# Performance work log

Measured on AMD Instinct MI355X. Metric: run time of the kernel, lower is better.

## Reference

```python
import jax, jax.numpy as jnp
import numpy as np

N_LAYERS = 4
D_MODEL = 1024
HEADS = 16
D_HEAD = D_MODEL // HEADS
SEQ = 1024
VOCAB = 512
FF = 4 * D_MODEL
MEM_LEN = 512
CMEM_LEN = 128
MAX_KLEN = SEQ + MEM_LEN + CMEM_LEN
BATCH = 4
LN_EPS = 1e-5
NEG = -1000000000.0


def shift(x):
    # Music-Transformer skew trick, faithful to torch shift()
    *lead, i, j = x.shape
    x = jnp.concatenate([x, jnp.zeros((*lead, i, i), x.dtype)], axis=-1)
    l = i + j - 1
    x = x.reshape(*lead, -1)
    pad = (-x.shape[-1]) % l
    x = jnp.concatenate([x, jnp.zeros((*lead, pad), x.dtype)], axis=-1)
    x = x.reshape(*lead, -1, l)
    return x[..., :i, i - 1:]


def layer_norm(x, g, b):
    mu = jnp.mean(x, axis=-1, keepdims=True)
    var = jnp.mean(jnp.square(x - mu), axis=-1, keepdims=True)
    return (x - mu) * jax.lax.rsqrt(var + LN_EPS) * g + b


def setup_inputs() -> dict:
    key = jax.random.key(0)
    ks = jax.random.split(key, 12)
    s = 0.02
    return {
        'seq': jax.random.randint(ks[0], (BATCH, SEQ), 0, VOCAB),
        'mask': jnp.ones((BATCH, SEQ), dtype=bool),
        'cmems': jnp.zeros((N_LAYERS, BATCH, CMEM_LEN, D_MODEL), jnp.float32),
        'mems': jnp.zeros((N_LAYERS, BATCH, MEM_LEN, D_MODEL), jnp.float32),
        'embed': jax.random.normal(ks[1], (VOCAB, D_MODEL), jnp.float32) * s,
        'Wq': jax.random.normal(ks[2], (N_LAYERS, D_MODEL, D_MODEL), jnp.float32) * s,
        'Wk': jax.random.normal(ks[3], (N_LAYERS, D_MODEL, D_MODEL), jnp.float32) * s,
        'Wv': jax.random.normal(ks[4], (N_LAYERS, D_MODEL, D_MODEL), jnp.float32) * s,
        'Wo': jax.random.normal(ks[5], (N_LAYERS, D_MODEL, D_MODEL), jnp.float32) * s,
        'r_emb': jax.random.normal(ks[6], (N_LAYERS, HEADS, MAX_KLEN, D_HEAD), jnp.float32) * s,
        'r_w_bias': jax.random.normal(ks[7], (N_LAYERS, HEADS, D_HEAD), jnp.float32) * s,
        'r_bias': jax.random.normal(ks[8], (N_LAYERS, HEADS, MAX_KLEN), jnp.float32) * s,
        'ln1_g': jnp.ones((N_LAYERS, D_MODEL), jnp.float32),
        'ln1_b': jnp.zeros((N_LAYERS, D_MODEL), jnp.float32),
        'ln2_g': jnp.ones((N_LAYERS, D_MODEL), jnp.float32),
        'ln2_b': jnp.zeros((N_LAYERS, D_MODEL), jnp.float32),
        'w1': jax.random.normal(ks[9], (N_LAYERS, FF, D_MODEL), jnp.float32) * s,
        'b1': jnp.zeros((N_LAYERS, FF), jnp.float32),
        'w2': jax.random.normal(ks[10], (N_LAYERS, D_MODEL, FF), jnp.float32) * s,
        'b2': jnp.zeros((N_LAYERS, D_MODEL), jnp.float32),
    }


def reference(seq, mask, cmems, mems, embed, Wq, Wk, Wv, Wo, r_emb,
              r_w_bias, r_bias, ln1_g, ln1_b, ln2_g, ln2_b, w1, b1, w2, b2):
    # Note: Encoder.forward passes memories=None to each layer, so cmems/mems
    # are unused, ar_loss == 0, and k_len == seq_len (faithful to source).
    B, S = seq.shape
    x = embed[seq]  # [B, S, D]
    # mask: [B,S] -> pairwise [B,1,S,S]
    m4 = (mask[:, :, None] & mask[:, None, :])[:, None]
    scale = HEADS ** -0.5  # source uses 1/sqrt(h), not 1/sqrt(d_head)

    def heads_split(y):  # [B,S,D] -> [B,H,S,dh]
        return y.reshape(B, S, HEADS, D_HEAD).transpose(0, 2, 1, 3)

    for i in range(N_LAYERS):
        q = heads_split(x @ Wq[i].T)
        k = heads_split(x @ Wk[i].T)
        v = heads_split(x @ Wv[i].T)
        re = r_emb[i][:, -S:, :]    # [H, S, dh]
        rb = r_bias[i][:, -S:]      # [H, S]
        r_query = q + r_w_bias[i][None, :, None, :]
        AC = jnp.einsum('bhid,bhjd->bhij', r_query, k)
        B_ = jnp.einsum('bhid,hjd->bhij', q, re)
        BD = shift(B_ + rb[None, :, None, :])
        score = (AC + BD) * scale
        score = jnp.where(m4, score, NEG)
        attn = jax.nn.softmax(score, axis=-1)
        out = jnp.einsum('bhij,bhjd->bhid', attn, v)
        out = out.transpose(0, 2, 1, 3).reshape(B, S, D_MODEL) @ Wo[i].T
        x = layer_norm(x + out, ln1_g[i], ln1_b[i])
        ff = jax.nn.gelu(x @ w1[i].T + b1[i], approximate=False) @ w2[i].T + b2[i]
        x = layer_norm(x + ff, ln2_g[i], ln2_b[i])
    return x
```

## Files before the change

kernel.cpp:

```cpp
#include <hip/hip_runtime.h>
#include <stdint.h>

#define DM 1024
#define NH 16
#define DH 64
#define SQ 1024
#define NB 4
#define FFD 4096
#define MAXK 1664
#define ROWS 4096
#define L2E 1.4426950408889634f

typedef __attribute__((ext_vector_type(8))) short short8;
typedef __attribute__((ext_vector_type(4))) float f32x4;

static __device__ __forceinline__ unsigned short f2bf(float f) {
    unsigned u = __float_as_uint(f);
    return (unsigned short)((u + 0x7fffu + ((u >> 16) & 1u)) >> 16);
}
static __device__ __forceinline__ float bf2f(unsigned short s) {
    return __uint_as_float(((unsigned)s) << 16);
}

__global__ __launch_bounds__(256) void k_embed(const int* __restrict__ seq,
                                               const float* __restrict__ emb,
                                               float* __restrict__ x,
                                               unsigned short* __restrict__ xb) {
    const int row = blockIdx.x, t = threadIdx.x;
    const int tok = seq[row];
    const float4 v = *(const float4*)(emb + (long)tok * DM + t * 4);
    *(float4*)(x + (long)row * DM + t * 4) = v;
    ushort4 o; o.x = f2bf(v.x); o.y = f2bf(v.y); o.z = f2bf(v.z); o.w = f2bf(v.w);
    *(ushort4*)(xb + (long)row * DM + t * 4) = o;
}

__global__ __launch_bounds__(256) void k_reb(const float* __restrict__ re,
                                             unsigned short* __restrict__ reb) {
    const long e = ((long)blockIdx.x * 256 + threadIdx.x) * 4;
    const int d = (int)(e & 63);
    const long rem = e >> 6;
    const int j = (int)(rem & 1023);
    const long lh = rem >> 10;
    const float4 v = *(const float4*)(re + (lh * MAXK + 640 + j) * DH + d);
    ushort4 o; o.x = f2bf(v.x); o.y = f2bf(v.y); o.z = f2bf(v.z); o.w = f2bf(v.w);
    *(ushort4*)(reb + e) = o;
}

__global__ __launch_bounds__(256) void k_ln(float* __restrict__ x,
                                            unsigned short* __restrict__ xb,
                                            const float* __restrict__ gw,
                                            const float* __restrict__ bw) {
    const int row = blockIdx.x, t = threadIdx.x;
    float4 v = *(const float4*)(x + (long)row * DM + t * 4);
    float s = v.x + v.y + v.z + v.w;
    float sq = v.x * v.x + v.y * v.y + v.z * v.z + v.w * v.w;
#pragma unroll
    for (int mk = 1; mk < 64; mk <<= 1) { s += __shfl_xor(s, mk); sq += __shfl_xor(sq, mk); }
    __shared__ float red[8];
    if ((t & 63) == 0) { red[(t >> 6) * 2] = s; red[(t >> 6) * 2 + 1] = sq; }
    __syncthreads();
    const float ts = red[0] + red[2] + red[4] + red[6];
    const float tq = red[1] + red[3] + red[5] + red[7];
    const float mu = ts * (1.f / DM);
    const float rstd = rsqrtf(tq * (1.f / DM) - mu * mu + 1e-5f);
    const float4 g4 = *(const float4*)(gw + t * 4);
    const float4 b4 = *(const float4*)(bw + t * 4);
    float4 o;
    o.x = (v.x - mu) * rstd * g4.x + b4.x;
    o.y = (v.y - mu) * rstd * g4.y + b4.y;
    o.z = (v.z - mu) * rstd * g4.z + b4.z;
    o.w = (v.w - mu) * rstd * g4.w + b4.w;
    *(float4*)(x + (long)row * DM + t * 4) = o;
    ushort4 ob; ob.x = f2bf(o.x); ob.y = f2bf(o.y); ob.z = f2bf(o.z); ob.w = f2bf(o.w);
    *(ushort4*)(xb + (long)row * DM + t * 4) = ob;
}

template <int MT, int EPI>
__global__ __launch_bounds__(256) void k_gemm(
    const unsigned short* __restrict__ A,
    const float* __restrict__ B0, const float* __restrict__ B1, const float* __restrict__ B2,
    const int K, const int N,
    float* __restrict__ xres, const float* __restrict__ bias,
    unsigned short* __restrict__ d0, unsigned short* __restrict__ d1,
    unsigned short* __restrict__ d2) {
    constexpr int BMv = MT * 32;
    __shared__ unsigned short As[BMv * 40];
    __shared__ unsigned short Bs[128 * 40];
    const int t = threadIdx.x;
    const int w = t >> 6, l = t & 63, g = l >> 4, c = l & 15;
    const int z = blockIdx.z;
    const float* Bw = (z == 0) ? B0 : ((z == 1) ? B1 : B2);
    const long m0 = (long)blockIdx.y * BMv, n0 = (long)blockIdx.x * 128;
    const int arow = (MT == 4) ? (t >> 1) : (t >> 2);
    const int aseg = (MT == 4) ? ((t & 1) * 16) : ((t & 3) * 8);
    const int brow = t >> 1, bseg = (t & 1) * 16;
    const unsigned short* asrc = A + (m0 + arow) * K + aseg;
    const float* bsrc = Bw + (n0 + brow) * K + bseg;
    f32x4 acc[MT][4];
#pragma unroll
    for (int i = 0; i < MT; i++)
#pragma unroll
        for (int j = 0; j < 4; j++) acc[i][j] = (f32x4){0.f, 0.f, 0.f, 0.f};
    const int wr = (w >> 1) * (MT * 16), wc = (w & 1) * 64;

    for (int kt = 0; kt < K; kt += 32) {
        uint4 a0, a1;
        a0 = *(const uint4*)(asrc + kt);
        if constexpr (MT == 4) a1 = *(const uint4*)(asrc + kt + 8);
        float4 f0 = *(const float4*)(bsrc + kt);
        float4 f1 = *(const float4*)(bsrc + kt + 4);
        float4 f2 = *(const float4*)(bsrc + kt + 8);
        float4 f3 = *(const float4*)(bsrc + kt + 12);
        *(uint4*)&As[arow * 40 + aseg] = a0;
        if constexpr (MT == 4) *(uint4*)&As[arow * 40 + aseg + 8] = a1;
        ushort4 u0, u1, u2, u3;
        u0.x = f2bf(f0.x); u0.y = f2bf(f0.y); u0.z = f2bf(f0.z); u0.w = f2bf(f0.w);
        u1.x = f2bf(f1.x); u1.y = f2bf(f1.y); u1.z = f2bf(f1.z); u1.w = f2bf(f1.w);
        u2.x = f2bf(f2.x); u2.y = f2bf(f2.y); u2.z = f2bf(f2.z); u2.w = f2bf(f2.w);
        u3.x = f2bf(f3.x); u3.y = f2bf(f3.y); u3.z = f2bf(f3.z); u3.w = f2bf(f3.w);
        *(ushort4*)&Bs[brow * 40 + bseg] = u0;
        *(ushort4*)&Bs[brow * 40 + bseg + 4] = u1;
        *(ushort4*)&Bs[brow * 40 + bseg + 8] = u2;
        *(ushort4*)&Bs[brow * 40 + bseg + 12] = u3;
        __syncthreads();
        short8 aF[MT], bF[4];
#pragma unroll
        for (int i = 0; i < MT; i++) aF[i] = *(const short8*)&As[(wr + i * 16 + c) * 40 + g * 8];
#pragma unroll
        for (int j = 0; j < 4; j++) bF[j] = *(const short8*)&Bs[(wc + j * 16 + c) * 40 + g * 8];
#pragma unroll
        for (int i = 0; i < MT; i++)
#pragma unroll
            for (int j = 0; j < 4; j++)
                acc[i][j] = __builtin_amdgcn_mfma_f32_16x16x32_bf16(aF[i], bF[j], acc[i][j], 0, 0, 0);
        __syncthreads();
    }

#pragma unroll
    for (int i = 0; i < MT; i++) {
#pragma unroll
        for (int j = 0; j < 4; j++) {
            const long ncol = n0 + wc + j * 16 + c;
            float bval = 0.f;
            if (EPI != 0) bval = (bias != nullptr) ? bias[ncol] : 0.f;
#pragma unroll
            for (int r = 0; r < 4; r++) {
                const long mrow = m0 + wr + i * 16 + g * 4 + r;
                const float vv = acc[i][j][r];
                if (EPI == 0) {
                    const long bb = mrow >> 10, ss = mrow & 1023, hh = ncol >> 6, dd = ncol & 63;
                    if (z == 0)      d0[((bb * NH + hh) * SQ + ss) * DH + dd] = f2bf(vv);
                    else if (z == 1) d1[((bb * NH + hh) * SQ + ss) * DH + dd] = f2bf(vv);
                    else             d2[((bb * NH + hh) * DH + dd) * SQ + ss] = f2bf(vv);
                } else if (EPI == 1) {
                    xres[mrow * DM + ncol] += vv + bval;
                } else {
                    const float xg = vv + bval;
                    d0[mrow * (long)N + ncol] = f2bf(0.5f * xg * (1.f + erff(xg * 0.70710678118654752f)));
                }
            }
        }
    }
}

__global__ __launch_bounds__(256) void k_attn(
    const unsigned short* __restrict__ q, const unsigned short* __restrict__ k,
    const unsigned short* __restrict__ vt, const unsigned short* __restrict__ reb,
    const float* __restrict__ rb, const float* __restrict__ rwb,
    unsigned short* __restrict__ ao) {
    const int t = threadIdx.x, w = t >> 6, l = t & 63, g = l >> 4, c = l & 15;
    const int bh = blockIdx.x, b = bh >> 4, h = bh & 15;
    const int q_base = blockIdx.y * 64 + w * 16;

    __shared__ float rb_s[SQ];
    __shared__ unsigned short p_s[4][640];
    for (int i = t; i < SQ; i += 256) rb_s[i] = rb[h * MAXK + 640 + i];
    __syncthreads();

    const unsigned short* qp = q + ((long)bh * SQ + q_base) * DH;
    const unsigned short* kp = k + (long)bh * SQ * DH;
    const unsigned short* vp = vt + (long)bh * DH * SQ;
    const unsigned short* rp = reb + (long)h * SQ * DH;

    short8 qf[2], qrf[2];
#pragma unroll
    for (int kk = 0; kk < 2; kk++) {
        qf[kk] = *(const short8*)(qp + c * DH + kk * 32 + g * 8);
        short8 tmp;
#pragma unroll
        for (int e = 0; e < 8; e++) {
            float vq = bf2f((unsigned short)qf[kk][e]) + rwb[h * DH + kk * 32 + g * 8 + e];
            tmp[e] = (short)f2bf(vq);
        }
        qrf[kk] = tmp;
    }

    f32x4 O[4];
    float mrow[4], lrow[4];
#pragma unroll
    for (int r = 0; r < 4; r++) { mrow[r] = -1e30f; lrow[r] = 0.f; }
#pragma unroll
    for (int dt = 0; dt < 4; dt++) O[dt] = (f32x4){0.f, 0.f, 0.f, 0.f};

    for (int kt = 0; kt < SQ / 32; kt++) {
        const int k0 = kt * 32;
        f32x4 ac[2];
#pragma unroll
        for (int tt = 0; tt < 2; tt++) {
            short8 kf0 = *(const short8*)(kp + (k0 + tt * 16 + c) * DH + g * 8);
            short8 kf1 = *(const short8*)(kp + (k0 + tt * 16 + c) * DH + 32 + g * 8);
            f32x4 zz = (f32x4){0.f, 0.f, 0.f, 0.f};
            zz = __builtin_amdgcn_mfma_f32_16x16x32_bf16(qrf[0], kf0, zz, 0, 0, 0);
            zz = __builtin_amdgcn_mfma_f32_16x16x32_bf16(qrf[1], kf1, zz, 0, 0, 0);
            ac[tt] = zz;
        }
        const int jb = k0 - q_base + SQ - 16;
        f32x4 G[3];
#pragma unroll
        for (int t2 = 0; t2 < 3; t2++) {
            int jr = jb + t2 * 16 + c;
            int jcl = jr < 0 ? 0 : (jr > SQ - 1 ? SQ - 1 : jr);
            short8 g0 = *(const short8*)(rp + (long)jcl * DH + g * 8);
            short8 g1 = *(const short8*)(rp + (long)jcl * DH + 32 + g * 8);
            f32x4 zz = (f32x4){0.f, 0.f, 0.f, 0.f};
            zz = __builtin_amdgcn_mfma_f32_16x16x32_bf16(qf[0], g0, zz, 0, 0, 0);
            zz = __builtin_amdgcn_mfma_f32_16x16x32_bf16(qf[1], g1, zz, 0, 0, 0);
            const float rbv = rb_s[jcl];
#pragma unroll
            for (int r = 0; r < 4; r++) zz[r] += rbv;
            G[t2] = zz;
        }
        float sc[2][4];
#pragma unroll
        for (int tt = 0; tt < 2; tt++) {
#pragma unroll
            for (int r = 0; r < 4; r++) {
                const int qi = g * 4 + r;
                const int ki = tt * 16 + c;
                const int mm = ki - qi + 15;
                const int sl = (l & 48) | (mm & 15);
                const float glo = __shfl(G[tt][r], sl, 64);
                const float ghi = __shfl(G[tt + 1][r], sl, 64);
                const float gsel = ((mm >> 4) == tt) ? glo : ghi;
                const bool valid = (k0 + ki) <= (q_base + qi);
                sc[tt][r] = (ac[tt][r] + (valid ? gsel : 0.f)) * 0.25f;
            }
        }
        float corr[4];
#pragma unroll
        for (int r = 0; r < 4; r++) {
            float v = fmaxf(sc[0][r], sc[1][r]);
            v = fmaxf(v, __shfl_xor(v, 1)); v = fmaxf(v, __shfl_xor(v, 2));
            v = fmaxf(v, __shfl_xor(v, 4)); v = fmaxf(v, __shfl_xor(v, 8));
            const float mn = fmaxf(mrow[r], v);
            corr[r] = exp2f((mrow[r] - mn) * L2E);
            const float p0 = exp2f((sc[0][r] - mn) * L2E);
            const float p1 = exp2f((sc[1][r] - mn) * L2E);
            float ps = p0 + p1;
            ps += __shfl_xor(ps, 1); ps += __shfl_xor(ps, 2);
            ps += __shfl_xor(ps, 4); ps += __shfl_xor(ps, 8);
            lrow[r] = lrow[r] * corr[r] + ps;
            mrow[r] = mn;
            p_s[w][(g * 4 + r) * 40 + c] = f2bf(p0);
            p_s[w][(g * 4 + r) * 40 + 16 + c] = f2bf(p1);
        }
#pragma unroll
        for (int dt = 0; dt < 4; dt++)
#pragma unroll
            for (int r = 0; r < 4; r++) O[dt][r] *= corr[r];
        __syncthreads();
        const short8 pf = *(const short8*)&p_s[w][c * 40 + g * 8];
#pragma unroll
        for (int dt = 0; dt < 4; dt++) {
            short8 vf = *(const short8*)(vp + (dt * 16 + c) * SQ + k0 + g * 8);
            O[dt] = __builtin_amdgcn_mfma_f32_16x16x32_bf16(pf, vf, O[dt], 0, 0, 0);
        }
    }

#pragma unroll
    for (int r = 0; r < 4; r++) {
        const float rl = 1.f / lrow[r];
        const int s = q_base + g * 4 + r;
#pragma unroll
        for (int dt = 0; dt < 4; dt++) {
            ao[((long)(b * SQ + s)) * DM + h * DH + dt * 16 + c] = f2bf(O[dt][r] * rl);
        }
    }
}

extern "C" void kernel_launch(void* const* d_in, const int* in_sizes, int n_in,
                              void* d_out, int out_size, void* d_ws, size_t ws_size,
                              hipStream_t stream) {
    const int* seq = (const int*)d_in[0];
    const float* emb = (const float*)d_in[4];
    const float* Wq = (const float*)d_in[5];
    const float* Wk = (const float*)d_in[6];
    const float* Wv = (const float*)d_in[7];
    const float* Wo = (const float*)d_in[8];
    const float* remb = (const float*)d_in[9];
    const float* rwb = (const float*)d_in[10];
    const float* rbias = (const float*)d_in[11];
    const float* ln1g = (const float*)d_in[12];
    const float* ln1b = (const float*)d_in[13];
    const float* ln2g = (const float*)d_in[14];
    const float* ln2b = (const float*)d_in[15];
    const float* w1 = (const float*)d_in[16];
    const float* b1 = (const float*)d_in[17];
    const float* w2 = (const float*)d_in[18];
    const float* b2 = (const float*)d_in[19];

    float* x = (float*)d_out;
    char* ws = (char*)d_ws;
    unsigned short* xb  = (unsigned short*)(ws);
    unsigned short* qb  = (unsigned short*)(ws + (8l  << 20));
    unsigned short* kb  = (unsigned short*)(ws + (16l << 20));
    unsigned short* vtb = (unsigned short*)(ws + (24l << 20));
    unsigned short* aob = (unsigned short*)(ws + (32l << 20));
    unsigned short* rebb = (unsigned short*)(ws + (40l << 20));
    unsigned short* hbb = (unsigned short*)(ws + (48l << 20));

    k_embed<<<dim3(ROWS), dim3(256), 0, stream>>>(seq, emb, x, xb);
    k_reb<<<dim3(4096), dim3(256), 0, stream>>>(remb, rebb);

    for (int i = 0; i < 4; i++) {
        const long wOff = (long)i * DM * DM;
        k_gemm<2, 0><<<dim3(8, 64, 3), dim3(256), 0, stream>>>(
            xb, Wq + wOff, Wk + wOff, Wv + wOff, DM, DM, nullptr, nullptr, qb, kb, vtb);
        k_attn<<<dim3(64, 16), dim3(256), 0, stream>>>(
            qb, kb, vtb, rebb + (long)i * NH * SQ * DH, rbias + (long)i * NH * MAXK,
            rwb + (long)i * NH * DH, aob);
        k_gemm<2, 1><<<dim3(8, 64, 1), dim3(256), 0, stream>>>(
            aob, Wo + wOff, nullptr, nullptr, DM, DM, x, nullptr, nullptr, nullptr, nullptr);
        k_ln<<<dim3(ROWS), dim3(256), 0, stream>>>(x, xb, ln1g + i * DM, ln1b + i * DM);
        k_gemm<4, 2><<<dim3(32, 32, 1), dim3(256), 0, stream>>>(
            xb, w1 + (long)i * FFD * DM, nullptr, nullptr, DM, FFD, nullptr,
            b1 + (long)i * FFD, hbb, nullptr, nullptr);
        k_gemm<2, 1><<<dim3(8, 64, 1), dim3(256), 0, stream>>>(
            hbb, w2 + (long)i * DM * FFD, nullptr, nullptr, FFD, DM, x,
            b2 + (long)i * DM, nullptr, nullptr, nullptr);
        k_ln<<<dim3(ROWS), dim3(256), 0, stream>>>(x, xb, ln2g + i * DM, ln2b + i * DM);
    }
}
```

Measured before the change: 2.766 ms.

## Pre-convert weights to bf16, use direct-to-LDS GEMM loads, widen attention tiles

Weights are converted to bf16 in separate kernels before each GEMM, and the fp32 weight conversion is removed from the GEMM inner loop. The GEMM now uses a uniform 128x128 tile and loads A and B with global_load_lds straight into unpadded shared memory. The attention kernel processes 64 keys per iteration instead of 32 and drops a block-wide barrier before reading P. The extra conversion launches and unpadded LDS rows can add traffic and bank conflicts. Workspace buffers are reused for the converted weights, which relies on the order of kernels on the stream.

```diff
diff --git a/kernel.cpp b/kernel.cpp
--- a/kernel.cpp
+++ b/kernel.cpp
@@ -13,6 +13,7 @@
 
 typedef __attribute__((ext_vector_type(8))) short short8;
 typedef __attribute__((ext_vector_type(4))) float f32x4;
+typedef unsigned int u32;
 
 static __device__ __forceinline__ unsigned short f2bf(float f) {
     unsigned u = __float_as_uint(f);
@@ -20,6 +21,10 @@
 }
 static __device__ __forceinline__ float bf2f(unsigned short s) {
     return __uint_as_float(((unsigned)s) << 16);
+}
+static __device__ __forceinline__ void gl16(const void* g, void* l) {
+    __builtin_amdgcn_global_load_lds((const __attribute__((address_space(1))) u32*)g,
+                                     (__attribute__((address_space(3))) u32*)l, 16, 0, 0);
 }
 
 __global__ __launch_bounds__(256) void k_embed(const int* __restrict__ seq,
@@ -44,6 +49,32 @@
     const float4 v = *(const float4*)(re + (lh * MAXK + 640 + j) * DH + d);
     ushort4 o; o.x = f2bf(v.x); o.y = f2bf(v.y); o.z = f2bf(v.z); o.w = f2bf(v.w);
     *(ushort4*)(reb + e) = o;
+}
+
+__global__ __launch_bounds__(256) void k_cvt(const float* __restrict__ s,
+                                             unsigned short* __restrict__ d, int n) {
+    const long i = ((long)blockIdx.x * 256 + threadIdx.x) * 8;
+    if (i >= n) return;
+    const float4 a = *(const float4*)(s + i);
+    const float4 b = *(const float4*)(s + i + 4);
+    ushort4 o0, o1;
+    o0.x = f2bf(a.x); o0.y = f2bf(a.y); o0.z = f2bf(a.z); o0.w = f2bf(a.w);
+    o1.x = f2bf(b.x); o1.y = f2bf(b.y); o1.z = f2bf(b.z); o1.w = f2bf(b.w);
+    *(ushort4*)(d + i) = o0; *(ushort4*)(d + i + 4) = o1;
+}
+__global__ __launch_bounds__(256) void k_cvt3(const float* __restrict__ s0,
+                                              const float* __restrict__ s1,
+                                              const float* __restrict__ s2,
+                                              unsigned short* __restrict__ d) {
+    const float* s = (blockIdx.z == 0) ? s0 : ((blockIdx.z == 1) ? s1 : s2);
+    const long i = ((long)blockIdx.x * 256 + threadIdx.x) * 8;
+    const float4 a = *(const float4*)(s + i);
+    const float4 b = *(const float4*)(s + i + 4);
+    ushort4 o0, o1;
+    o0.x = f2bf(a.x); o0.y = f2bf(a.y); o0.z = f2bf(a.z); o0.w = f2bf(a.w);
+    o1.x = f2bf(b.x); o1.y = f2bf(b.y); o1.z = f2bf(b.z); o1.w = f2bf(b.w);
+    unsigned short* dz = d + (long)blockIdx.z * (DM * DM);
+    *(ushort4*)(dz + i) = o0; *(ushort4*)(dz + i + 4) = o1;
 }
 
 __global__ __launch_bounds__(256) void k_ln(float* __restrict__ x,
@@ -75,61 +106,50 @@
     *(ushort4*)(xb + (long)row * DM + t * 4) = ob;
 }
 
-template <int MT, int EPI>
+template <int EPI>
 __global__ __launch_bounds__(256) void k_gemm(
-    const unsigned short* __restrict__ A,
-    const float* __restrict__ B0, const float* __restrict__ B1, const float* __restrict__ B2,
+    const unsigned short* __restrict__ A, const unsigned short* __restrict__ B,
     const int K, const int N,
     float* __restrict__ xres, const float* __restrict__ bias,
     unsigned short* __restrict__ d0, unsigned short* __restrict__ d1,
     unsigned short* __restrict__ d2) {
-    constexpr int BMv = MT * 32;
-    __shared__ unsigned short As[BMv * 40];
-    __shared__ unsigned short Bs[128 * 40];
+    __shared__ unsigned short As[128 * 32];
+    __shared__ unsigned short Bs[128 * 32];
     const int t = threadIdx.x;
     const int w = t >> 6, l = t & 63, g = l >> 4, c = l & 15;
     const int z = blockIdx.z;
-    const float* Bw = (z == 0) ? B0 : ((z == 1) ? B1 : B2);
-    const long m0 = (long)blockIdx.y * BMv, n0 = (long)blockIdx.x * 128;
-    const int arow = (MT == 4) ? (t >> 1) : (t >> 2);
-    const int aseg = (MT == 4) ? ((t & 1) * 16) : ((t & 3) * 8);
-    const int brow = t >> 1, bseg = (t & 1) * 16;
-    const unsigned short* asrc = A + (m0 + arow) * K + aseg;
-    const float* bsrc = Bw + (n0 + brow) * K + bseg;
-    f32x4 acc[MT][4];
-#pragma unroll
-    for (int i = 0; i < MT; i++)
+    const unsigned short* Bw = B + (long)z * ((long)N * K);
+    const long m0 = (long)blockIdx.y * 128, n0 = (long)blockIdx.x * 128;
+    const int lrow = l >> 2, lseg = (l & 3) << 3;
+    const unsigned short* ag0 = A + (m0 + (w * 2 + 0) * 16 + lrow) * (long)K + lseg;
+    const unsigned short* ag1 = A + (m0 + (w * 2 + 1) * 16 + lrow) * (long)K + lseg;
+    const unsigned short* bg0 = Bw + (n0 + (w * 2 + 0) * 16 + lrow) * (long)K + lseg;
+    const unsigned short* bg1 = Bw + (n0 + (w * 2 + 1) * 16 + lrow) * (long)K + lseg;
+    unsigned short* al0 = &As[(w * 2 + 0) * 512];
+    unsigned short* al1 = &As[(w * 2 + 1) * 512];
+    unsigned short* bl0 = &Bs[(w * 2 + 0) * 512];
+    unsigned short* bl1 = &Bs[(w * 2 + 1) * 512];
+
+    f32x4 acc[4][4];
+#pragma unroll
+    for (int i = 0; i < 4; i++)
 #pragma unroll
         for (int j = 0; j < 4; j++) acc[i][j] = (f32x4){0.f, 0.f, 0.f, 0.f};
-    const int wr = (w >> 1) * (MT * 16), wc = (w & 1) * 64;
+    const int wr = (w >> 1) * 64, wc = (w & 1) * 64;
 
     for (int kt = 0; kt < K; kt += 32) {
-        uint4 a0, a1;
-        a0 = *(const uint4*)(asrc + kt);
-        if constexpr (MT == 4) a1 = *(const uint4*)(asrc + kt + 8);
-        float4 f0 = *(const float4*)(bsrc + kt);
-        float4 f1 = *(const float4*)(bsrc + kt + 4);
-        float4 f2 = *(const float4*)(bsrc + kt + 8);
-        float4 f3 = *(const float4*)(bsrc + kt + 12);
-        *(uint4*)&As[arow * 40 + aseg] = a0;
-        if constexpr (MT == 4) *(uint4*)&As[arow * 40 + aseg + 8] = a1;
-        ushort4 u0, u1, u2, u3;
-        u0.x = f2bf(f0.x); u0.y = f2bf(f0.y); u0.z = f2bf(f0.z); u0.w = f2bf(f0.w);
-        u1.x = f2bf(f1.x); u1.y = f2bf(f1.y); u1.z = f2bf(f1.z); u1.w = f2bf(f1.w);
-        u2.x = f2bf(f2.x); u2.y = f2bf(f2.y); u2.z = f2bf(f2.z); u2.w = f2bf(f2.w);
-        u3.x = f2bf(f3.x); u3.y = f2bf(f3.y); u3.z = f2bf(f3.z); u3.w = f2bf(f3.w);
-        *(ushort4*)&Bs[brow * 40 + bseg] = u0;
-        *(ushort4*)&Bs[brow * 40 + bseg + 4] = u1;
-        *(ushort4*)&Bs[brow * 40 + bseg + 8] = u2;
-        *(ushort4*)&Bs[brow * 40 + bseg + 12] = u3;
+        gl16(ag0 + kt, al0);
+        gl16(ag1 + kt, al1);
+        gl16(bg0 + kt, bl0);
+        gl16(bg1 + kt, bl1);
         __syncthreads();
-        short8 aF[MT], bF[4];
-#pragma unroll
-        for (int i = 0; i < MT; i++) aF[i] = *(const short8*)&As[(wr + i * 16 + c) * 40 + g * 8];
-#pragma unroll
-        for (int j = 0; j < 4; j++) bF[j] = *(const short8*)&Bs[(wc + j * 16 + c) * 40 + g * 8];
-#pragma unroll
-        for (int i = 0; i < MT; i++)
+        short8 aF[4], bF[4];
+#pragma unroll
+        for (int i = 0; i < 4; i++) aF[i] = *(const short8*)&As[(wr + i * 16 + c) * 32 + g * 8];
+#pragma unroll
+        for (int j = 0; j < 4; j++) bF[j] = *(const short8*)&Bs[(wc + j * 16 + c) * 32 + g * 8];
+#pragma unroll
+        for (int i = 0; i < 4; i++)
 #pragma unroll
             for (int j = 0; j < 4; j++)
                 acc[i][j] = __builtin_amdgcn_mfma_f32_16x16x32_bf16(aF[i], bF[j], acc[i][j], 0, 0, 0);
@@ -137,7 +157,7 @@
     }
 
 #pragma unroll
-    for (int i = 0; i < MT; i++) {
+    for (int i = 0; i < 4; i++) {
 #pragma unroll
         for (int j = 0; j < 4; j++) {
             const long ncol = n0 + wc + j * 16 + c;
@@ -173,7 +193,7 @@
     const int q_base = blockIdx.y * 64 + w * 16;
 
     __shared__ float rb_s[SQ];
-    __shared__ unsigned short p_s[4][640];
+    __shared__ unsigned short p_s[4][16 * 72];
     for (int i = t; i < SQ; i += 256) rb_s[i] = rb[h * MAXK + 640 + i];
     __syncthreads();
 
@@ -202,11 +222,11 @@
 #pragma unroll
     for (int dt = 0; dt < 4; dt++) O[dt] = (f32x4){0.f, 0.f, 0.f, 0.f};
 
-    for (int kt = 0; kt < SQ / 32; kt++) {
-        const int k0 = kt * 32;
-        f32x4 ac[2];
-#pragma unroll
-        for (int tt = 0; tt < 2; tt++) {
+    for (int kt = 0; kt < SQ / 64; kt++) {
+        const int k0 = kt * 64;
+        f32x4 ac[4];
+#pragma unroll
+        for (int tt = 0; tt < 4; tt++) {
             short8 kf0 = *(const short8*)(kp + (k0 + tt * 16 + c) * DH + g * 8);
             short8 kf1 = *(const short8*)(kp + (k0 + tt * 16 + c) * DH + 32 + g * 8);
             f32x4 zz = (f32x4){0.f, 0.f, 0.f, 0.f};
@@ -215,9 +235,9 @@
             ac[tt] = zz;
         }
         const int jb = k0 - q_base + SQ - 16;
-        f32x4 G[3];
-#pragma unroll
-        for (int t2 = 0; t2 < 3; t2++) {
+        f32x4 G[5];
+#pragma unroll
+        for (int t2 = 0; t2 < 5; t2++) {
             int jr = jb + t2 * 16 + c;
             int jcl = jr < 0 ? 0 : (jr > SQ - 1 ? SQ - 1 : jr);
             short8 g0 = *(const short8*)(rp + (long)jcl * DH + g * 8);
@@ -230,9 +250,9 @@
             for (int r = 0; r < 4; r++) zz[r] += rbv;
             G[t2] = zz;
         }
-        float sc[2][4];
-#pragma unroll
-        for (int tt = 0; tt < 2; tt++) {
+        float sc[4][4];
+#pragma unroll
+        for (int tt = 0; tt < 4; tt++) {
 #pragma unroll
             for (int r = 0; r < 4; r++) {
                 const int qi = g * 4 + r;
@@ -240,7 +260,7 @@
                 const int mm = ki - qi + 15;
                 const int sl = (l & 48) | (mm & 15);
                 const float glo = __shfl(G[tt][r], sl, 64);
-                const float ghi = __shfl(G[tt + 1][r], sl, 64);
+                const float ghi = __shfl(G[tt + 1 < 5 ? tt + 1 : 4][r], sl, 64);
                 const float gsel = ((mm >> 4) == tt) ? glo : ghi;
                 const bool valid = (k0 + ki) <= (q_base + qi);
                 sc[tt][r] = (ac[tt][r] + (valid ? gsel : 0.f)) * 0.25f;
@@ -249,31 +269,38 @@
         float corr[4];
 #pragma unroll
         for (int r = 0; r < 4; r++) {
-            float v = fmaxf(sc[0][r], sc[1][r]);
+            float v = fmaxf(fmaxf(sc[0][r], sc[1][r]), fmaxf(sc[2][r], sc[3][r]));
             v = fmaxf(v, __shfl_xor(v, 1)); v = fmaxf(v, __shfl_xor(v, 2));
             v = fmaxf(v, __shfl_xor(v, 4)); v = fmaxf(v, __shfl_xor(v, 8));
             const float mn = fmaxf(mrow[r], v);
             corr[r] = exp2f((mrow[r] - mn) * L2E);
-            const float p0 = exp2f((sc[0][r] - mn) * L2E);
-            const float p1 = exp2f((sc[1][r] - mn) * L2E);
-            float ps = p0 + p1;
+            float p0 = exp2f((sc[0][r] - mn) * L2E);
+            float p1 = exp2f((sc[1][r] - mn) * L2E);
+            float p2 = exp2f((sc[2][r] - mn) * L2E);
+            float p3 = exp2f((sc[3][r] - mn) * L2E);
+            float ps = (p0 + p1) + (p2 + p3);
             ps += __shfl_xor(ps, 1); ps += __shfl_xor(ps, 2);
             ps += __shfl_xor(ps, 4); ps += __shfl_xor(ps, 8);
             lrow[r] = lrow[r] * corr[r] + ps;
             mrow[r] = mn;
-            p_s[w][(g * 4 + r) * 40 + c] = f2bf(p0);
-            p_s[w][(g * 4 + r) * 40 + 16 + c] = f2bf(p1);
+            const int prow = (g * 4 + r) * 72;
+            p_s[w][prow + c] = f2bf(p0);
+            p_s[w][prow + 16 + c] = f2bf(p1);
+            p_s[w][prow + 32 + c] = f2bf(p2);
+            p_s[w][prow + 48 + c] = f2bf(p3);
         }
 #pragma unroll
         for (int dt = 0; dt < 4; dt++)
 #pragma unroll
             for (int r = 0; r < 4; r++) O[dt][r] *= corr[r];
-        __syncthreads();
-        const short8 pf = *(const short8*)&p_s[w][c * 40 + g * 8];
+        const short8 pf0 = *(const short8*)&p_s[w][c * 72 + g * 8];
+        const short8 pf1 = *(const short8*)&p_s[w][c * 72 + 32 + g * 8];
 #pragma unroll
         for (int dt = 0; dt < 4; dt++) {
-            short8 vf = *(const short8*)(vp + (dt * 16 + c) * SQ + k0 + g * 8);
-            O[dt] = __builtin_amdgcn_mfma_f32_16x16x32_bf16(pf, vf, O[dt], 0, 0, 0);
+            short8 vf0 = *(const short8*)(vp + (dt * 16 + c) * SQ + k0 + g * 8);
+            short8 vf1 = *(const short8*)(vp + (dt * 16 + c) * SQ + k0 + 32 + g * 8);
+            O[dt] = __builtin_amdgcn_mfma_f32_16x16x32_bf16(pf0, vf0, O[dt], 0, 0, 0);
+            O[dt] = __builtin_amdgcn_mfma_f32_16x16x32_bf16(pf1, vf1, O[dt], 0, 0, 0);
         }
     }
 
@@ -311,33 +338,39 @@
 
     float* x = (float*)d_out;
     char* ws = (char*)d_ws;
-    unsigned short* xb  = (unsigned short*)(ws);
-    unsigned short* qb  = (unsigned short*)(ws + (8l  << 20));
-    unsigned short* kb  = (unsigned short*)(ws + (16l << 20));
-    unsigned short* vtb = (unsigned short*)(ws + (24l << 20));
-    unsigned short* aob = (unsigned short*)(ws + (32l << 20));
+    unsigned short* xb   = (unsigned short*)(ws);
+    unsigned short* qb   = (unsigned short*)(ws + (8l << 20));
+    unsigned short* kb   = (unsigned short*)(ws + (16l << 20));
+    unsigned short* vtb  = (unsigned short*)(ws + (24l << 20));
+    unsigned short* aob  = (unsigned short*)(ws + (32l << 20));
     unsigned short* rebb = (unsigned short*)(ws + (40l << 20));
-    unsigned short* hbb = (unsigned short*)(ws + (48l << 20));
+    unsigned short* hbb  = (unsigned short*)(ws + (48l << 20));
+    unsigned short* wqkv = aob;
+    unsigned short* wo_b = qb;
+    unsigned short* w1_b = kb;
+    unsigned short* w2_b = vtb;
 
     k_embed<<<dim3(ROWS), dim3(256), 0, stream>>>(seq, emb, x, xb);
     k_reb<<<dim3(4096), dim3(256), 0, stream>>>(remb, rebb);
 
     for (int i = 0; i < 4; i++) {
         const long wOff = (long)i * DM * DM;
-        k_gemm<2, 0><<<dim3(8, 64, 3), dim3(256), 0, stream>>>(
-            xb, Wq + wOff, Wk + wOff, Wv + wOff, DM, DM, nullptr, nullptr, qb, kb, vtb);
+        k_cvt3<<<dim3(512, 1, 3), dim3(256), 0, stream>>>(Wq + wOff, Wk + wOff, Wv + wOff, wqkv);
+        k_gemm<0><<<dim3(8, 32, 3), dim3(256), 0, stream>>>(
+            xb, wqkv, DM, DM, nullptr, nullptr, qb, kb, vtb);
         k_attn<<<dim3(64, 16), dim3(256), 0, stream>>>(
             qb, kb, vtb, rebb + (long)i * NH * SQ * DH, rbias + (long)i * NH * MAXK,
             rwb + (long)i * NH * DH, aob);
-        k_gemm<2, 1><<<dim3(8, 64, 1), dim3(256), 0, stream>>>(
-            aob, Wo + wOff, nullptr, nullptr, DM, DM, x, nullptr, nullptr, nullptr, nullptr);
+        k_cvt<<<dim3(512), dim3(256), 0, stream>>>(Wo + wOff, wo_b, DM * DM);
+        k_gemm<1><<<dim3(8, 32, 1), dim3(256), 0, stream>>>(
+            aob, wo_b, DM, DM, x, nullptr, nullptr, nullptr, nullptr);
         k_ln<<<dim3(ROWS), dim3(256), 0, stream>>>(x, xb, ln1g + i * DM, ln1b + i * DM);
-        k_gemm<4, 2><<<dim3(32, 32, 1), dim3(256), 0, stream>>>(
-            xb, w1 + (long)i * FFD * DM, nullptr, nullptr, DM, FFD, nullptr,
-            b1 + (long)i * FFD, hbb, nullptr, nullptr);
-        k_gemm<2, 1><<<dim3(8, 64, 1), dim3(256), 0, stream>>>(
-            hbb, w2 + (long)i * DM * FFD, nullptr, nullptr, FFD, DM, x,
-            b2 + (long)i * DM, nullptr, nullptr, nullptr);
+        k_cvt<<<dim3(2048), dim3(256), 0, stream>>>(w1 + (long)i * FFD * DM, w1_b, FFD * DM);
+        k_gemm<2><<<dim3(32, 32, 1), dim3(256), 0, stream>>>(
+            xb, w1_b, DM, FFD, nullptr, b1 + (long)i * FFD, hbb, nullptr, nullptr);
+        k_cvt<<<dim3(2048), dim3(256), 0, stream>>>(w2 + (long)i * DM * FFD, w2_b, DM * FFD);
+        k_gemm<1><<<dim3(8, 32, 1), dim3(256), 0, stream>>>(
+            hbb, w2_b, FFD, DM, x, b2 + (long)i * DM, nullptr, nullptr, nullptr);
         k_ln<<<dim3(ROWS), dim3(256), 0, stream>>>(x, xb, ln2g + i * DM, ln2b + i * DM);
     }
 }
```

Result: faster. 2.273 ms (-17.8%).
